# Kernel tuning notes

Hardware: AMD Instinct MI355X
Metric: run time of the kernel (lower is better)

Reference implementation:

```python
import jax, jax.numpy as jnp
import numpy as np

NUM_HEADS = 16


def rotate_half(x):
    x1 = x[..., ::2]
    x2 = x[..., 1::2]
    return jnp.concatenate((-x2, x1), axis=-1)


def rope_sin_cos(seq_len, head_dim, dtype):
    inv_freq = 1.0 / (10000.0 ** (jnp.arange(0, head_dim, 2, dtype=jnp.float32) / head_dim))
    t = jnp.arange(seq_len, dtype=jnp.float32)
    freqs = jnp.einsum('i,j->ij', t, inv_freq)          # [S, D/2]
    emb = jnp.concatenate((freqs, freqs), axis=-1)      # [S, D]
    return jnp.sin(emb).astype(dtype), jnp.cos(emb).astype(dtype)


def setup_inputs() -> dict:
    key = jax.random.key(0)
    B, S, E = 2, 2048, 2048
    ks = jax.random.split(key, 5)
    scale = 1.0 / np.sqrt(E)
    return {
        'x': jax.random.normal(ks[0], (B, S, E), dtype=jnp.float32),
        'mask': jnp.ones((B, S), dtype=jnp.int32),
        'Wq': jax.random.normal(ks[1], (E, E), dtype=jnp.float32) * scale,
        'bq': jnp.zeros((E,), dtype=jnp.float32),
        'Wk': jax.random.normal(ks[2], (E, E), dtype=jnp.float32) * scale,
        'bk': jnp.zeros((E,), dtype=jnp.float32),
        'Wv': jax.random.normal(ks[3], (E, E), dtype=jnp.float32) * scale,
        'bv': jnp.zeros((E,), dtype=jnp.float32),
        'Wo': jax.random.normal(ks[4], (E, E), dtype=jnp.float32) * scale,
        'bo': jnp.zeros((E,), dtype=jnp.float32),
    }


def reference(x, mask, Wq, bq, Wk, bk, Wv, bv, Wo, bo):
    B, S, E = x.shape
    H = NUM_HEADS
    D = E // H
    q = (x @ Wq + bq).reshape(B, S, H, D).transpose(0, 2, 1, 3)  # [B,H,S,D]
    k = (x @ Wk + bk).reshape(B, S, H, D).transpose(0, 2, 1, 3)
    v = (x @ Wv + bv).reshape(B, S, H, D).transpose(0, 2, 1, 3)

    sin, cos = rope_sin_cos(S, D, q.dtype)  # [S,D]
    sin = sin[None, None]                    # [1,1,S,D]
    cos = cos[None, None]
    q = q * cos + rotate_half(q) * sin
    k = k * cos + rotate_half(k) * sin

    scores = jnp.einsum('bhqd,bhkd->bhqk', q, k) / jnp.sqrt(jnp.asarray(D, q.dtype))
    scores = jnp.where(mask[:, None, None, :] == 0, -jnp.inf, scores)
    probs = jax.nn.softmax(scores, axis=-1)
    attn = jnp.einsum('bhqk,bhkd->bhqd', probs, v)       # [B,H,S,D]
    attn = attn.transpose(0, 2, 1, 3).reshape(B, S, E)
    return attn @ Wo + bo
```

## Files before the change

### kernel.cpp

```cpp
#include <hip/hip_runtime.h>
#include <hip/hip_bf16.h>
#include <cmath>

typedef unsigned short u16;
typedef unsigned int   u32;

using v4f    = __attribute__((ext_vector_type(4)))  float;
using f32x16 = __attribute__((ext_vector_type(16))) float;
using s8v    = __attribute__((ext_vector_type(8)))  short;
using u32x2  = __attribute__((ext_vector_type(2)))  unsigned int;

union Frag { uint4 u; s8v s; };

__device__ __forceinline__ u16 f2bf(float f){
  u32 u = __float_as_uint(f);
  u32 r = u + 0x7fffu + ((u >> 16) & 1u);
  return (u16)(r >> 16);
}
__device__ __forceinline__ float bf2f(u16 h){ return __uint_as_float(((u32)h) << 16); }

__device__ __forceinline__ u32 cvtpk(float a, float b){
  u32 r;
  asm("v_cvt_pk_bf16_f32 %0, %1, %2" : "=v"(r) : "v"(a), "v"(b));
  return r;
}

__device__ __forceinline__ void async16(const void* g, void* l){
  __builtin_amdgcn_global_load_lds((__attribute__((address_space(1))) void*)g,
                                   (__attribute__((address_space(3))) void*)l, 16, 0, 0);
}

__global__ __launch_bounds__(256) void prep_kernel(
    const float* __restrict__ x, u16* __restrict__ xb,
    const float* __restrict__ W0, const float* __restrict__ W1,
    const float* __restrict__ W2, const float* __restrict__ W3,
    u16* __restrict__ T0, u16* __restrict__ T1, u16* __restrict__ T2, u16* __restrict__ T3){
  __shared__ float tile[64][65];
  const int bid = blockIdx.x;
  if (bid < 8192){
    size_t i = ((size_t)bid * 256 + threadIdx.x) * 4;
    float4 v = *(const float4*)(x + i);
    uint2 o;
    o.x = (u32)f2bf(v.x) | ((u32)f2bf(v.y) << 16);
    o.y = (u32)f2bf(v.z) | ((u32)f2bf(v.w) << 16);
    *(uint2*)(xb + i) = o;
    return;
  }
  const int t4 = bid - 8192;
  const int z  = t4 >> 10;
  const float* W = (z==0)?W0:(z==1)?W1:(z==2)?W2:W3;
  u16*         T = (z==0)?T0:(z==1)?T1:(z==2)?T2:T3;
  const int k0 = ((t4 & 1023) >> 5)*64, n0 = (t4 & 31)*64;
  const int t  = threadIdx.x;
  const int rr = t >> 4, c4 = (t & 15) * 4;
  #pragma unroll
  for (int i=0;i<4;i++){
    int k = rr + i*16;
    float4 v = *(const float4*)(W + (size_t)(k0+k)*2048 + n0 + c4);
    tile[k][c4+0]=v.x; tile[k][c4+1]=v.y; tile[k][c4+2]=v.z; tile[k][c4+3]=v.w;
  }
  __syncthreads();
  #pragma unroll
  for (int i=0;i<4;i++){
    int n = rr + i*16;
    uint2 o;
    o.x = (u32)f2bf(tile[c4+0][n]) | ((u32)f2bf(tile[c4+1][n])<<16);
    o.y = (u32)f2bf(tile[c4+2][n]) | ((u32)f2bf(tile[c4+3][n])<<16);
    *(uint2*)(T + (size_t)(n0+n)*2048 + k0 + c4) = o;
  }
}

template<int MODE>
__device__ __forceinline__ void gemm_tile(const u16* __restrict__ A, const u16* __restrict__ BT,
                                          const float* __restrict__ bias, void* __restrict__ Cout,
                                          int m0, int n0, u16* sm){
  constexpr int K = 2048;
  u16* Asl = sm;
  u16* Bsl = sm + 8192;
  const int tid  = threadIdx.x;
  const int w    = tid >> 6;
  const int lane = tid & 63;
  const int r    = lane & 15, q = lane >> 4;
  const int wm   = (w >> 1) * 64, wn = (w & 1) * 64;

  v4f acc[4][4];
  #pragma unroll
  for (int i=0;i<4;i++)
    #pragma unroll
    for (int j=0;j<4;j++) acc[i][j] = (v4f)0.f;

  const int srow = w*32 + (lane>>3);
  const int sblk = (lane&7) ^ ((lane>>3)&7);
  const u16* Ag = A  + (size_t)(m0+srow)*K + sblk*8;
  const u16* Bg = BT + (size_t)(n0+srow)*K + sblk*8;
  u16* Als = Asl + (w*32)*64;
  u16* Bls = Bsl + (w*32)*64;

  for (int kk = 0; kk < K; kk += 64) {
    #pragma unroll
    for (int i=0;i<4;i++){
      async16(Ag + (size_t)i*8*K + kk, Als + i*512);
      async16(Bg + (size_t)i*8*K + kk, Bls + i*512);
    }
    __syncthreads();
    #pragma unroll
    for (int ks=0; ks<2; ++ks) {
      s8v af[4], bfr[4];
      #pragma unroll
      for (int i=0;i<4;i++){
        int rho = wm + i*16 + r;
        int p = (ks*4 + q) ^ (r&7);
        Frag t; t.u = *(const uint4*)(Asl + rho*64 + p*8); af[i] = t.s;
      }
      #pragma unroll
      for (int j=0;j<4;j++){
        int rho = wn + j*16 + r;
        int p = (ks*4 + q) ^ (r&7);
        Frag t; t.u = *(const uint4*)(Bsl + rho*64 + p*8); bfr[j] = t.s;
      }
      #pragma unroll
      for (int i=0;i<4;i++)
        #pragma unroll
        for (int j=0;j<4;j++)
          acc[i][j] = __builtin_amdgcn_mfma_f32_16x16x32_bf16(af[i], bfr[j], acc[i][j], 0, 0, 0);
    }
    __syncthreads();
  }

  float bv[4];
  #pragma unroll
  for (int j=0;j<4;j++) bv[j] = bias[n0 + wn + j*16 + r];

  if constexpr (MODE != 3){
    #pragma unroll
    for (int i=0;i<4;i++){
      #pragma unroll
      for (int j=0;j<4;j++){
        const int gn = n0 + wn + j*16 + r;
        #pragma unroll
        for (int rr2=0; rr2<4; ++rr2){
          const int gm = m0 + wm + i*16 + q*4 + rr2;
          float val = acc[i][j][rr2] + bv[j];
          if (MODE == 0) ((u16*)Cout)[(size_t)gm*2048 + gn] = f2bf(val);
          else           ((float*)Cout)[(size_t)gm*2048 + gn] = val;
        }
      }
    }
  } else {
    #pragma unroll
    for (int i=0;i<4;i++)
      #pragma unroll
      for (int j=0;j<4;j++){
        const int col = wn + j*16 + r;
        #pragma unroll
        for (int rr2=0; rr2<4; ++rr2)
          sm[(wm + i*16 + q*4 + rr2)*128 + col] = f2bf(acc[i][j][rr2] + bv[j]);
      }
    __syncthreads();
    const float invf = exp2f(-(float)lane * 0.20762050593045952f);
    for (int rr=0; rr<32; ++rr){
      const int row = w*32 + rr;
      const int s = (m0 + row) & 2047;
      float sn, cs;
      sincosf((float)s * invf, &sn, &cs);
      const u16* tr = sm + row*128;
      float x_j   = bf2f(tr[lane]);
      float x_j64 = bf2f(tr[64 + lane]);
      float x_2j  = bf2f(tr[2*lane]);
      float x_2j1 = bf2f(tr[2*lane + 1]);
      u16* gp = (u16*)Cout + (size_t)(m0 + row)*2048 + n0;
      gp[lane]      = f2bf(x_j  * cs - x_2j1 * sn);
      gp[64 + lane] = f2bf(x_j64 * cs + x_2j  * sn);
    }
  }
}

__global__ __launch_bounds__(256) void gemm_qkv_kernel(
    const u16* __restrict__ A,
    const u16* __restrict__ WqT, const u16* __restrict__ WkT, const u16* __restrict__ WvT,
    const float* __restrict__ bq, const float* __restrict__ bk, const float* __restrict__ bv,
    u16* __restrict__ Qb, u16* __restrict__ Kb, u16* __restrict__ Vb){
  __shared__ u16 sm[16384];
  const int bx = blockIdx.x, by = blockIdx.y;
  const int mat = bx >> 4;
  const u16*   BT   = (mat==0)?WqT:(mat==1)?WkT:WvT;
  const float* bias = (mat==0)?bq :(mat==1)?bk :bv;
  u16*         Cout = (mat==0)?Qb :(mat==1)?Kb :Vb;
  if (mat < 2) gemm_tile<3>(A, BT, bias, Cout, by*128, (bx & 15)*128, sm);
  else         gemm_tile<0>(A, BT, bias, Cout, by*128, (bx & 15)*128, sm);
}

__global__ __launch_bounds__(256) void gemm_wo_kernel(const u16* __restrict__ A,
                                                      const u16* __restrict__ WoT,
                                                      const float* __restrict__ bias,
                                                      float* __restrict__ out){
  __shared__ u16 sm[16384];
  gemm_tile<1>(A, WoT, bias, out, blockIdx.y*128, blockIdx.x*128, sm);
}

__global__ __launch_bounds__(256) void tv_kernel(const u16* __restrict__ V, u16* __restrict__ VT){
  __shared__ u16 t[64*72];
  const int tb = blockIdx.x;
  const int s0 = (tb & 31)*64;
  const int d0 = ((tb >> 5) & 1)*64;
  const int bh = tb >> 6;
  const int b = bh >> 4, h = bh & 15;
  const size_t obase = ((size_t)bh*128 + d0)*2048 + s0;
  const int tid = threadIdx.x;
  #pragma unroll
  for (int i=0;i<2;i++){
    int c = tid + i*256;
    int sl = c >> 3, dc = (c & 7) * 8;
    *(uint4*)(t + sl*72 + dc) =
      *(const uint4*)(V + ((size_t)(b*2048 + s0 + sl))*2048 + h*128 + d0 + dc);
  }
  __syncthreads();
  #pragma unroll
  for (int i=0;i<2;i++){
    int c = tid + i*256;
    int dl = c >> 3, sc4 = (c & 7) * 8;
    u16 tmp[8];
    #pragma unroll
    for (int j=0;j<8;j++) tmp[j] = t[(sc4+j)*72 + dl];
    *(uint4*)(VT + obase + (size_t)dl*2048 + sc4) = *(const uint4*)tmp;
  }
}

__global__ __launch_bounds__(256,2) void attn_kernel(const u16* __restrict__ Q,
                                                     const u16* __restrict__ K,
                                                     const u16* __restrict__ VT,
                                                     const int* __restrict__ mask,
                                                     u16* __restrict__ Out){
  constexpr int S = 2048;
  constexpr float SL2 = 0.08838834764831845f * 1.4426950408889634f;
  __shared__ u16 smem[32768];

  const int tid = threadIdx.x, w = tid >> 6, lane = tid & 63;
  const int qc = lane & 31;
  const int h  = lane >> 5;
  const int l7 = lane & 7;
  const int hh = blockIdx.y, b = blockIdx.z;
  const int q0 = blockIdx.x * 128;
  const size_t rowb = (size_t)b * 2048;
  const size_t bhD  = ((size_t)(b*16 + hh)) * 128;

  s8v qf[8];
  {
    const u16* qp = Q + (rowb + q0 + w*32 + qc)*2048 + hh*128 + h*8;
    #pragma unroll
    for (int t=0;t<8;t++){ Frag f; f.u = *(const uint4*)(qp + t*16); qf[t] = f.s; }
  }

  f32x16 accO[4];
  #pragma unroll
  for (int d=0; d<4; d++) accO[d] = (f32x16)0.f;
  float lsum = 0.f;

  const int sr4 = lane >> 4, sp16 = lane & 15;
  const int vr8 = lane >> 3, vp8 = lane & 7;

  auto stage = [&](u16* base, int key0){
    u16* Kd = base;
    u16* Vd = base + 8192;
    #pragma unroll
    for (int i=0;i<4;i++){
      int R = w*16 + i*4;
      int ob = sp16 ^ ((R&7) + sr4);
      async16(K + (rowb + key0 + R + sr4)*2048 + hh*128 + ob*8, Kd + R*128);
    }
    #pragma unroll
    for (int i=0;i<4;i++){
      int R = w*32 + i*8;
      int ob = vp8 ^ vr8;
      async16(VT + (bhD + R + vr8)*2048 + key0 + ob*8, Vd + R*64);
    }
  };

  stage(smem, 0);
  int mv = mask[b*S + lane];
  __syncthreads();
  unsigned long long bm = __ballot(mv != 0);
  int cur = 0;

  for (int it=0; it<32; ++it){
    if (it < 31){
      stage(smem + (cur^1)*16384, (it+1)*64);
      mv = mask[b*S + (it+1)*64 + lane];
    }
    const u16* Ks = smem + cur*16384;
    const u16* Vs = Ks + 8192;

    #pragma unroll
    for (int nb=0; nb<2; ++nb){
      f32x16 sc = (f32x16)0.f;
      __builtin_amdgcn_s_setprio(1);
      #pragma unroll
      for (int t=0;t<8;t++){
        Frag kf; kf.u = *(const uint4*)(Ks + (nb*32 + qc)*128 + (((2*t + h) ^ l7)*8));
        sc = __builtin_amdgcn_mfma_f32_32x32x16_bf16(kf.s, qf[t], sc, 0, 0, 0);
      }
      __builtin_amdgcn_s_setprio(0);
      float p[16];
      #pragma unroll
      for (int m=0; m<16; ++m) p[m] = exp2f(sc[m] * SL2);
      if (bm != ~0ull){
        #pragma unroll
        for (int m=0; m<16; ++m){
          int bit = nb*32 + (m&3) + 8*(m>>2) + 4*h;
          if (!((bm >> bit) & 1ull)) p[m] = 0.f;
        }
      }
      #pragma unroll
      for (int m=0; m<16; ++m) lsum += p[m];

      #pragma unroll
      for (int g=0; g<2; ++g){
        u32 a0 = cvtpk(p[8*g+0], p[8*g+1]);
        u32 a1 = cvtpk(p[8*g+2], p[8*g+3]);
        u32 a2 = cvtpk(p[8*g+4], p[8*g+5]);
        u32 a3 = cvtpk(p[8*g+6], p[8*g+7]);
        u32x2 r0 = __builtin_amdgcn_permlane32_swap(a0, a2, false, false);
        u32x2 r1 = __builtin_amdgcn_permlane32_swap(a1, a3, false, false);
        Frag pf; pf.u = make_uint4(r0[0], r1[0], r0[1], r1[1]);
        const int T = nb*2 + g;
        __builtin_amdgcn_s_setprio(1);
        #pragma unroll
        for (int d=0; d<4; ++d){
          Frag vf; vf.u = *(const uint4*)(Vs + (d*32 + qc)*64 + (((2*T + h) ^ l7)*8));
          accO[d] = __builtin_amdgcn_mfma_f32_32x32x16_bf16(vf.s, pf.s, accO[d], 0, 0, 0);
        }
        __builtin_amdgcn_s_setprio(0);
      }
    }
    __syncthreads();
    bm = __ballot(mv != 0);
    cur ^= 1;
  }

  float sall = lsum + __shfl_xor(lsum, 32, 64);
  float invv = (sall > 0.f) ? 1.f/sall : 0.f;
  u16* orow = Out + (rowb + q0 + w*32 + qc)*2048 + hh*128;
  #pragma unroll
  for (int d=0; d<4; ++d){
    #pragma unroll
    for (int g2=0; g2<4; ++g2){
      uint2 o;
      o.x = cvtpk(accO[d][g2*4+0] * invv, accO[d][g2*4+1] * invv);
      o.y = cvtpk(accO[d][g2*4+2] * invv, accO[d][g2*4+3] * invv);
      *(uint2*)(orow + d*32 + g2*8 + 4*h) = o;
    }
  }
}

extern "C" void kernel_launch(void* const* d_in, const int* in_sizes, int n_in,
                              void* d_out, int out_size, void* d_ws, size_t ws_size,
                              hipStream_t stream) {
  (void)in_sizes; (void)n_in; (void)out_size; (void)ws_size;
  const float* x    = (const float*)d_in[0];
  const int*   mask = (const int*)d_in[1];
  const float* Wq   = (const float*)d_in[2];
  const float* bq   = (const float*)d_in[3];
  const float* Wk   = (const float*)d_in[4];
  const float* bk   = (const float*)d_in[5];
  const float* Wv   = (const float*)d_in[6];
  const float* bv   = (const float*)d_in[7];
  const float* Wo   = (const float*)d_in[8];
  const float* bo   = (const float*)d_in[9];

  u16* xbf = (u16*)d_ws;
  u16* WqT = xbf + 8388608;
  u16* WkT = WqT + 4194304;
  u16* WvT = WkT + 4194304;
  u16* WoT = WvT + 4194304;
  u16* Qb  = WoT + 4194304;
  u16* Kb  = Qb + 8388608;
  u16* Vb  = Kb + 8388608;
  u16* VTb = Vb + 8388608;
  u16* Ab  = VTb + 8388608;

  prep_kernel<<<12288, 256, 0, stream>>>(x, xbf, Wq, Wk, Wv, Wo, WqT, WkT, WvT, WoT);
  gemm_qkv_kernel<<<dim3(48,32), 256, 0, stream>>>(xbf, WqT, WkT, WvT, bq, bk, bv, Qb, Kb, Vb);
  tv_kernel<<<2048, 256, 0, stream>>>(Vb, VTb);
  attn_kernel<<<dim3(16,16,2), 256, 0, stream>>>(Qb, Kb, VTb, mask, Ab);
  gemm_wo_kernel<<<dim3(16,32), 256, 0, stream>>>(Ab, WoT, bo, (float*)d_out);
}
```

Measured before the change: 404.3 us.

## Precompute RoPE sin/cos table in prep kernel and narrow Wo GEMM tiles

Adds a sin/cos table (2048x64 float2), built by extra blocks of the prep kernel and stored in the attention-output scratch buffer. The QKV GEMM epilogue then reads this table instead of calling sincosf for every row. The GEMM tile is also templated on N-width, and the Wo projection now uses 128x64 tiles, doubling its grid to 1024 blocks for better CU occupancy. In exchange the epilogue does an extra global load per row, and the Wo tiles reuse less data.

New measurement: 418.2 us. 3.4% more time.

```diff
diff --git a/kernel.cpp b/kernel.cpp
--- a/kernel.cpp
+++ b/kernel.cpp
@@ -34,7 +34,8 @@
     const float* __restrict__ x, u16* __restrict__ xb,
     const float* __restrict__ W0, const float* __restrict__ W1,
     const float* __restrict__ W2, const float* __restrict__ W3,
-    u16* __restrict__ T0, u16* __restrict__ T1, u16* __restrict__ T2, u16* __restrict__ T3){
+    u16* __restrict__ T0, u16* __restrict__ T1, u16* __restrict__ T2, u16* __restrict__ T3,
+    float2* __restrict__ tab){
   __shared__ float tile[64][65];
   const int bid = blockIdx.x;
   if (bid < 8192){
@@ -46,6 +47,15 @@
     *(uint2*)(xb + i) = o;
     return;
   }
+  if (bid >= 12288){
+    const int idx = (bid - 12288)*256 + threadIdx.x;
+    const int s = idx >> 6, j = idx & 63;
+    float invf = exp2f(-(float)j * 0.20762050593045952f);
+    float sn, cs;
+    sincosf((float)s * invf, &sn, &cs);
+    tab[idx] = make_float2(sn, cs);
+    return;
+  }
   const int t4 = bid - 8192;
   const int z  = t4 >> 10;
   const float* W = (z==0)?W0:(z==1)?W1:(z==2)?W2:W3;
@@ -70,10 +80,10 @@
   }
 }
 
-template<int MODE>
+template<int MODE, int NJ>
 __device__ __forceinline__ void gemm_tile(const u16* __restrict__ A, const u16* __restrict__ BT,
                                           const float* __restrict__ bias, void* __restrict__ Cout,
-                                          int m0, int n0, u16* sm){
+                                          int m0, int n0, u16* sm, const float2* __restrict__ tab){
   constexpr int K = 2048;
   u16* Asl = sm;
   u16* Bsl = sm + 8192;
@@ -81,31 +91,33 @@
   const int w    = tid >> 6;
   const int lane = tid & 63;
   const int r    = lane & 15, q = lane >> 4;
-  const int wm   = (w >> 1) * 64, wn = (w & 1) * 64;
-
-  v4f acc[4][4];
+  const int wm   = (w >> 1) * 64, wn = (w & 1) * (16*NJ);
+
+  v4f acc[4][NJ];
   #pragma unroll
   for (int i=0;i<4;i++)
     #pragma unroll
-    for (int j=0;j<4;j++) acc[i][j] = (v4f)0.f;
+    for (int j=0;j<NJ;j++) acc[i][j] = (v4f)0.f;
 
   const int srow = w*32 + (lane>>3);
+  const int brow = w*(8*NJ) + (lane>>3);
   const int sblk = (lane&7) ^ ((lane>>3)&7);
   const u16* Ag = A  + (size_t)(m0+srow)*K + sblk*8;
-  const u16* Bg = BT + (size_t)(n0+srow)*K + sblk*8;
+  const u16* Bg = BT + (size_t)(n0+brow)*K + sblk*8;
   u16* Als = Asl + (w*32)*64;
-  u16* Bls = Bsl + (w*32)*64;
+  u16* Bls = Bsl + (w*(8*NJ))*64;
 
   for (int kk = 0; kk < K; kk += 64) {
     #pragma unroll
-    for (int i=0;i<4;i++){
+    for (int i=0;i<4;i++)
       async16(Ag + (size_t)i*8*K + kk, Als + i*512);
+    #pragma unroll
+    for (int i=0;i<NJ;i++)
       async16(Bg + (size_t)i*8*K + kk, Bls + i*512);
-    }
     __syncthreads();
     #pragma unroll
     for (int ks=0; ks<2; ++ks) {
-      s8v af[4], bfr[4];
+      s8v af[4], bfr[NJ];
       #pragma unroll
       for (int i=0;i<4;i++){
         int rho = wm + i*16 + r;
@@ -113,7 +125,7 @@
         Frag t; t.u = *(const uint4*)(Asl + rho*64 + p*8); af[i] = t.s;
       }
       #pragma unroll
-      for (int j=0;j<4;j++){
+      for (int j=0;j<NJ;j++){
         int rho = wn + j*16 + r;
         int p = (ks*4 + q) ^ (r&7);
         Frag t; t.u = *(const uint4*)(Bsl + rho*64 + p*8); bfr[j] = t.s;
@@ -121,21 +133,21 @@
       #pragma unroll
       for (int i=0;i<4;i++)
         #pragma unroll
-        for (int j=0;j<4;j++)
+        for (int j=0;j<NJ;j++)
           acc[i][j] = __builtin_amdgcn_mfma_f32_16x16x32_bf16(af[i], bfr[j], acc[i][j], 0, 0, 0);
     }
     __syncthreads();
   }
 
-  float bv[4];
-  #pragma unroll
-  for (int j=0;j<4;j++) bv[j] = bias[n0 + wn + j*16 + r];
+  float bv[NJ];
+  #pragma unroll
+  for (int j=0;j<NJ;j++) bv[j] = bias[n0 + wn + j*16 + r];
 
   if constexpr (MODE != 3){
     #pragma unroll
     for (int i=0;i<4;i++){
       #pragma unroll
-      for (int j=0;j<4;j++){
+      for (int j=0;j<NJ;j++){
         const int gn = n0 + wn + j*16 + r;
         #pragma unroll
         for (int rr2=0; rr2<4; ++rr2){
@@ -150,27 +162,26 @@
     #pragma unroll
     for (int i=0;i<4;i++)
       #pragma unroll
-      for (int j=0;j<4;j++){
+      for (int j=0;j<NJ;j++){
         const int col = wn + j*16 + r;
         #pragma unroll
         for (int rr2=0; rr2<4; ++rr2)
           sm[(wm + i*16 + q*4 + rr2)*128 + col] = f2bf(acc[i][j][rr2] + bv[j]);
       }
     __syncthreads();
-    const float invf = exp2f(-(float)lane * 0.20762050593045952f);
+    #pragma unroll 8
     for (int rr=0; rr<32; ++rr){
       const int row = w*32 + rr;
       const int s = (m0 + row) & 2047;
-      float sn, cs;
-      sincosf((float)s * invf, &sn, &cs);
+      float2 sc2 = tab[s*64 + lane];
       const u16* tr = sm + row*128;
       float x_j   = bf2f(tr[lane]);
       float x_j64 = bf2f(tr[64 + lane]);
       float x_2j  = bf2f(tr[2*lane]);
       float x_2j1 = bf2f(tr[2*lane + 1]);
       u16* gp = (u16*)Cout + (size_t)(m0 + row)*2048 + n0;
-      gp[lane]      = f2bf(x_j  * cs - x_2j1 * sn);
-      gp[64 + lane] = f2bf(x_j64 * cs + x_2j  * sn);
+      gp[lane]      = f2bf(x_j  * sc2.y - x_2j1 * sc2.x);
+      gp[64 + lane] = f2bf(x_j64 * sc2.y + x_2j  * sc2.x);
     }
   }
 }
@@ -179,23 +190,24 @@
     const u16* __restrict__ A,
     const u16* __restrict__ WqT, const u16* __restrict__ WkT, const u16* __restrict__ WvT,
     const float* __restrict__ bq, const float* __restrict__ bk, const float* __restrict__ bv,
-    u16* __restrict__ Qb, u16* __restrict__ Kb, u16* __restrict__ Vb){
+    u16* __restrict__ Qb, u16* __restrict__ Kb, u16* __restrict__ Vb,
+    const float2* __restrict__ tab){
   __shared__ u16 sm[16384];
   const int bx = blockIdx.x, by = blockIdx.y;
   const int mat = bx >> 4;
   const u16*   BT   = (mat==0)?WqT:(mat==1)?WkT:WvT;
   const float* bias = (mat==0)?bq :(mat==1)?bk :bv;
   u16*         Cout = (mat==0)?Qb :(mat==1)?Kb :Vb;
-  if (mat < 2) gemm_tile<3>(A, BT, bias, Cout, by*128, (bx & 15)*128, sm);
-  else         gemm_tile<0>(A, BT, bias, Cout, by*128, (bx & 15)*128, sm);
+  if (mat < 2) gemm_tile<3,4>(A, BT, bias, Cout, by*128, (bx & 15)*128, sm, tab);
+  else         gemm_tile<0,4>(A, BT, bias, Cout, by*128, (bx & 15)*128, sm, tab);
 }
 
 __global__ __launch_bounds__(256) void gemm_wo_kernel(const u16* __restrict__ A,
                                                       const u16* __restrict__ WoT,
                                                       const float* __restrict__ bias,
                                                       float* __restrict__ out){
-  __shared__ u16 sm[16384];
-  gemm_tile<1>(A, WoT, bias, out, blockIdx.y*128, blockIdx.x*128, sm);
+  __shared__ u16 sm[12288];
+  gemm_tile<1,2>(A, WoT, bias, out, blockIdx.y*128, blockIdx.x*64, sm, nullptr);
 }
 
 __global__ __launch_bounds__(256) void tv_kernel(const u16* __restrict__ V, u16* __restrict__ VT){
@@ -377,10 +389,11 @@
   u16* Vb  = Kb + 8388608;
   u16* VTb = Vb + 8388608;
   u16* Ab  = VTb + 8388608;
-
-  prep_kernel<<<12288, 256, 0, stream>>>(x, xbf, Wq, Wk, Wv, Wo, WqT, WkT, WvT, WoT);
-  gemm_qkv_kernel<<<dim3(48,32), 256, 0, stream>>>(xbf, WqT, WkT, WvT, bq, bk, bv, Qb, Kb, Vb);
+  float2* tab = (float2*)Ab;
+
+  prep_kernel<<<12800, 256, 0, stream>>>(x, xbf, Wq, Wk, Wv, Wo, WqT, WkT, WvT, WoT, tab);
+  gemm_qkv_kernel<<<dim3(48,32), 256, 0, stream>>>(xbf, WqT, WkT, WvT, bq, bk, bv, Qb, Kb, Vb, tab);
   tv_kernel<<<2048, 256, 0, stream>>>(Vb, VTb);
   attn_kernel<<<dim3(16,16,2), 256, 0, stream>>>(Qb, Kb, VTb, mask, Ab);
-  gemm_wo_kernel<<<dim3(16,32), 256, 0, stream>>>(Ab, WoT, bo, (float*)d_out);
-}
+  gemm_wo_kernel<<<dim3(32,32), 256, 0, stream>>>(Ab, WoT, bo, (float*)d_out);
+}
```
